# Performance work log

Measured on AMD Instinct MI355X. Metric: run time of the kernel, lower is better.

The kernel has to match this reference:

```python
import jax, jax.numpy as jnp
import numpy as np


def _upsample2x_axis_ac(arr, axis):
    size_in = arr.shape[axis]
    size_out = 2 * size_in
    pos = jnp.arange(size_out, dtype=arr.dtype) * ((size_in - 1) / (size_out - 1))
    i0 = jnp.clip(jnp.floor(pos).astype(jnp.int32), 0, size_in - 2)
    w = pos - i0.astype(arr.dtype)
    a = jnp.take(arr, i0, axis=axis)
    b = jnp.take(arr, i0 + 1, axis=axis)
    bshape = [1] * arr.ndim
    bshape[axis] = size_out
    w = w.reshape(bshape)
    return a * (1 - w) + b * w


def setup_inputs() -> dict:
    key = jax.random.key(0)
    k1, k2, k3, k4 = jax.random.split(key, 4)
    B, C, H, W = 8, 64, 256, 256
    Cr = 128  # readout channels (>= C, topk selects C of them)
    x = jax.random.normal(k1, (B, C, H, W), dtype=jnp.float32)
    readout = jax.random.normal(k2, (B, Cr, H // 2, W // 2), dtype=jnp.float32)
    weight = jax.random.normal(k3, (C, 2, 1, 1), dtype=jnp.float32) * 0.5
    bias = jax.random.normal(k4, (C,), dtype=jnp.float32) * 0.1
    return {"x": x, "readout": readout, "weight": weight, "bias": bias}


def reference(x, readout, weight, bias):
    B, C, H, W = x.shape
    r = _upsample2x_axis_ac(readout, 2)
    r = _upsample2x_axis_ac(r, 3)  # [B, Cr, H, W]
    # 2) topk channel selection by global-average score
    scores = r.mean(axis=(2, 3))  # [B, Cr]
    _, idx = jax.lax.top_k(scores, C)  # [B, C]
    r = jnp.take_along_axis(r, idx[:, :, None, None], axis=1)  # [B, C, H, W]
    # 3) interleave + grouped 1x1 conv (groups=C): group c sees channels
    #    (2c, 2c+1) = (x_c, r_c); equivalent to per-channel affine mix.
    w0 = weight[:, 0, 0, 0][None, :, None, None]
    w1 = weight[:, 1, 0, 0][None, :, None, None]
    gate = jax.nn.sigmoid(x * w0 + r * w1 + bias[None, :, None, None])
    # 4) sigmoid-gated blend
    return x * (1 - gate) + r * gate
```

## Files before the change

kernel.cpp:

```cpp
#include <hip/hip_runtime.h>
#include <math.h>

constexpr int B_   = 8;
constexpr int C_   = 64;
constexpr int H_   = 256;
constexpr int W_   = 256;
constexpr int CR_  = 128;
constexpr int HIN_ = 128;
constexpr int WIN_ = 128;

typedef float f4v __attribute__((ext_vector_type(4)));
typedef float f4u __attribute__((ext_vector_type(4), aligned(4)));

__device__ __forceinline__ float kScale() { return 127.0f / 255.0f; }

__global__ __launch_bounds__(256) void scores_kernel(
    const float* __restrict__ readout, float* __restrict__ scores)
{
    __shared__ float cw[HIN_];
    __shared__ float red[256];
    const int t  = threadIdx.x;
    const int bc = blockIdx.x;

    if (t < HIN_) {
        float acc = 0.0f;
        const float s = kScale();
        int jlo = 2 * t - 3; if (jlo < 0) jlo = 0;
        int jhi = 2 * t + 3; if (jhi > H_ - 1) jhi = H_ - 1;
        for (int j = jlo; j <= jhi; ++j) {
            float pos = j * s;
            int i0 = (int)pos;
            if (i0 > HIN_ - 2) i0 = HIN_ - 2;
            float w = pos - (float)i0;
            if (i0 == t)     acc += (1.0f - w);
            if (i0 + 1 == t) acc += w;
        }
        cw[t] = acc * (1.0f / 256.0f);
    }
    __syncthreads();

    const int c4 = t & 31;
    const int rg = t >> 5;
    const f4v* base = (const f4v*)(readout + (size_t)bc * HIN_ * WIN_);

    f4v a4 = (f4v){0.f, 0.f, 0.f, 0.f};
    const int i0r = rg * 16;
#pragma unroll 4
    for (int i = i0r; i < i0r + 16; ++i) {
        const float cwi = cw[i];
        f4v v = base[i * (WIN_ / 4) + c4];
        a4 += cwi * v;
    }
    red[t] = a4.x * cw[4 * c4 + 0] + a4.y * cw[4 * c4 + 1] +
             a4.z * cw[4 * c4 + 2] + a4.w * cw[4 * c4 + 3];
    __syncthreads();
    for (int off = 128; off > 0; off >>= 1) {
        if (t < off) red[t] += red[t + off];
        __syncthreads();
    }
    if (t == 0) scores[bc] = red[0];
}

__global__ __launch_bounds__(CR_) void topk_kernel(
    const float* __restrict__ scores, int* __restrict__ idx)
{
    __shared__ float s[CR_];
    const int t = threadIdx.x;
    const int b = blockIdx.x;
    s[t] = scores[b * CR_ + t];
    __syncthreads();
    const float mine = s[t];
    int rank = 0;
    for (int o = 0; o < CR_; ++o) {
        float so = s[o];
        rank += (so > mine) || (so == mine && o < t);
    }
    if (rank < C_) idx[b * C_ + rank] = t;
}

__device__ __forceinline__ float sel_a(f4u w, int d) {
    return d == 0 ? w[0] : (d == 1 ? w[1] : w[2]);
}
__device__ __forceinline__ float sel_b(f4u w, int d) {
    return d == 0 ? w[1] : (d == 1 ? w[2] : w[3]);
}

__global__ __launch_bounds__(256) void fuse_kernel(
    const float* __restrict__ x, const float* __restrict__ readout,
    const float* __restrict__ weight, const float* __restrict__ bias,
    const int* __restrict__ idx, float* __restrict__ out)
{
    constexpr int RPB = 16;
    const int gid  = blockIdx.x;
    const int bc   = gid >> 4;
    const int hblk = gid & 15;
    const int tid  = threadIdx.x;
    const int rgrp = tid >> 6;
    const int lane = tid & 63;
    const int b = bc >> 6;
    const int c = bc & 63;

    const int rc    = idx[b * C_ + c];
    const float w0  = weight[c * 2 + 0];
    const float w1  = weight[c * 2 + 1];
    const float bsv = bias[c];

    const float s = kScale();

    int   j0c[4];
    float wx[4];
    const int wbase = lane * 4;
#pragma unroll
    for (int k = 0; k < 4; ++k) {
        float wpos = (wbase + k) * s;
        int j0 = (int)wpos;
        if (j0 > WIN_ - 2) j0 = WIN_ - 2;
        wx[k]  = wpos - (float)j0;
        j0c[k] = j0;
    }
    int j00 = j0c[0];
    if (j00 > WIN_ - 4) j00 = WIN_ - 4;

    const float* rbase = readout + ((size_t)b * CR_ + rc) * HIN_ * WIN_;
    const float* xrow0 = x   + (((size_t)bc) * H_ + hblk * RPB + rgrp) * W_;
    float*       orow0 = out + (((size_t)bc) * H_ + hblk * RPB + rgrp) * W_;

#pragma unroll
    for (int rr = 0; rr < 4; ++rr) {
        const int h = hblk * RPB + rr * 4 + rgrp;
        float hpos = h * s;
        int i0 = (int)hpos;
        if (i0 > HIN_ - 2) i0 = HIN_ - 2;
        const float wy = hpos - (float)i0;

        const float* r0 = rbase + (size_t)i0 * WIN_;
        const float* r1 = r0 + WIN_;

        const f4v* xin = (const f4v*)(xrow0 + (size_t)(rr * 4) * W_);
        f4v*       oo  = (f4v*)      (orow0 + (size_t)(rr * 4) * W_);

        const f4v xv  = __builtin_nontemporal_load(&xin[lane]);
        const f4u w0v = *(const f4u*)(r0 + j00);
        const f4u w1v = *(const f4u*)(r1 + j00);

        const float xf[4] = {xv.x, xv.y, xv.z, xv.w};
        f4v ov;
#pragma unroll
        for (int k = 0; k < 4; ++k) {
            const int d = j0c[k] - j00;
            float ta = sel_a(w0v, d), tb = sel_b(w0v, d);
            float ba = sel_a(w1v, d), bb = sel_b(w1v, d);
            float top = ta + wx[k] * (tb - ta);
            float bot = ba + wx[k] * (bb - ba);
            float rv  = top + wy * (bot - top);

            float z = xf[k] * w0 + rv * w1 + bsv;
            float g = 1.0f / (1.0f + __expf(-z));
            ov[k] = xf[k] + g * (rv - xf[k]);
        }
        __builtin_nontemporal_store(ov, &oo[lane]);
    }
}

extern "C" void kernel_launch(void* const* d_in, const int* in_sizes, int n_in,
                              void* d_out, int out_size, void* d_ws, size_t ws_size,
                              hipStream_t stream)
{
    const float* x       = (const float*)d_in[0];
    const float* readout = (const float*)d_in[1];
    const float* weight  = (const float*)d_in[2];
    const float* bias    = (const float*)d_in[3];
    float* out = (float*)d_out;

    float* scores = (float*)d_ws;
    int*   idx    = (int*)((char*)d_ws + B_ * CR_ * sizeof(float));

    scores_kernel<<<B_ * CR_, 256, 0, stream>>>(readout, scores);
    topk_kernel<<<B_, CR_, 0, stream>>>(scores, idx);
    fuse_kernel<<<B_ * C_ * (H_ / 16), 256, 0, stream>>>(x, readout, weight, bias, idx, out);
}
```

Baseline: 278.6 us.

## Fuse scores, topk and blend into one cooperative kernel with grid syncs

Merges the three kernels into a single cooperative launch of 1024 blocks that use grid.sync between the score, top-k and blend phases. This removes two kernel launch gaps. Each block now processes 8 row tiles in the blend phase instead of one, which reduces parallelism from 8192 blocks to 1024. It also adds the cost of grid-wide barriers, and it falls back to the old three-kernel path if the cooperative launch fails.

```diff
diff --git a/kernel.cpp b/kernel.cpp
--- a/kernel.cpp
+++ b/kernel.cpp
@@ -1,5 +1,8 @@
 #include <hip/hip_runtime.h>
+#include <hip/hip_cooperative_groups.h>
 #include <math.h>
+
+namespace cg = cooperative_groups;
 
 constexpr int B_   = 8;
 constexpr int C_   = 64;
@@ -13,6 +16,162 @@
 typedef float f4u __attribute__((ext_vector_type(4), aligned(4)));
 
 __device__ __forceinline__ float kScale() { return 127.0f / 255.0f; }
+
+__device__ __forceinline__ float sel_a(f4u w, int d) {
+    return d == 0 ? w[0] : (d == 1 ? w[1] : w[2]);
+}
+__device__ __forceinline__ float sel_b(f4u w, int d) {
+    return d == 0 ? w[1] : (d == 1 ? w[2] : w[3]);
+}
+
+__global__ __launch_bounds__(256, 4) void mega_kernel(
+    const float* __restrict__ x, const float* __restrict__ readout,
+    const float* __restrict__ weight, const float* __restrict__ bias,
+    float* __restrict__ out, float* __restrict__ scores, int* __restrict__ idx)
+{
+    cg::grid_group grid = cg::this_grid();
+    const int t = threadIdx.x;
+
+    {
+        __shared__ float cw[HIN_];
+        __shared__ float red[256];
+        const int bc = blockIdx.x;
+
+        if (t < HIN_) {
+            float acc = 0.0f;
+            const float s = kScale();
+            int jlo = 2 * t - 3; if (jlo < 0) jlo = 0;
+            int jhi = 2 * t + 3; if (jhi > H_ - 1) jhi = H_ - 1;
+            for (int j = jlo; j <= jhi; ++j) {
+                float pos = j * s;
+                int i0 = (int)pos;
+                if (i0 > HIN_ - 2) i0 = HIN_ - 2;
+                float w = pos - (float)i0;
+                if (i0 == t)     acc += (1.0f - w);
+                if (i0 + 1 == t) acc += w;
+            }
+            cw[t] = acc * (1.0f / 256.0f);
+        }
+        __syncthreads();
+
+        const int c4 = t & 31;
+        const int rg = t >> 5;
+        const f4v* base = (const f4v*)(readout + (size_t)bc * HIN_ * WIN_);
+
+        f4v a4 = (f4v){0.f, 0.f, 0.f, 0.f};
+        const int i0r = rg * 16;
+#pragma unroll 4
+        for (int i = i0r; i < i0r + 16; ++i) {
+            const float cwi = cw[i];
+            f4v v = base[i * (WIN_ / 4) + c4];
+            a4 += cwi * v;
+        }
+        red[t] = a4.x * cw[4 * c4 + 0] + a4.y * cw[4 * c4 + 1] +
+                 a4.z * cw[4 * c4 + 2] + a4.w * cw[4 * c4 + 3];
+        __syncthreads();
+        for (int off = 128; off > 0; off >>= 1) {
+            if (t < off) red[t] += red[t + off];
+            __syncthreads();
+        }
+        if (t == 0) scores[bc] = red[0];
+    }
+
+    grid.sync();
+
+    if (blockIdx.x < B_) {
+        __shared__ float s[CR_];
+        const int b = blockIdx.x;
+        if (t < CR_) s[t] = scores[b * CR_ + t];
+        __syncthreads();
+        if (t < CR_) {
+            const float mine = s[t];
+            int rank = 0;
+            for (int o = 0; o < CR_; ++o) {
+                float so = s[o];
+                rank += (so > mine) || (so == mine && o < t);
+            }
+            if (rank < C_) idx[b * C_ + rank] = t;
+        }
+    }
+
+    grid.sync();
+
+    {
+        constexpr int RPB = 16;
+        const int tile0 = blockIdx.x * 8;
+        const int bc    = tile0 >> 4;
+        const int hblk0 = tile0 & 15;
+        const int rgrp  = t >> 6;
+        const int lane  = t & 63;
+        const int b = bc >> 6;
+        const int c = bc & 63;
+
+        const int rc    = idx[b * C_ + c];
+        const float w0  = weight[c * 2 + 0];
+        const float w1  = weight[c * 2 + 1];
+        const float bsv = bias[c];
+
+        const float s = kScale();
+
+        int   j0c[4];
+        float wx[4];
+        const int wbase = lane * 4;
+#pragma unroll
+        for (int k = 0; k < 4; ++k) {
+            float wpos = (wbase + k) * s;
+            int j0 = (int)wpos;
+            if (j0 > WIN_ - 2) j0 = WIN_ - 2;
+            wx[k]  = wpos - (float)j0;
+            j0c[k] = j0;
+        }
+        int j00 = j0c[0];
+        if (j00 > WIN_ - 4) j00 = WIN_ - 4;
+
+        const float* rbase = readout + ((size_t)b * CR_ + rc) * HIN_ * WIN_;
+
+        for (int kt = 0; kt < 8; ++kt) {
+            const int hblk = hblk0 + kt;
+            const float* xrow0 = x   + (((size_t)bc) * H_ + hblk * RPB + rgrp) * W_;
+            float*       orow0 = out + (((size_t)bc) * H_ + hblk * RPB + rgrp) * W_;
+
+#pragma unroll
+            for (int rr = 0; rr < 4; ++rr) {
+                const int h = hblk * RPB + rr * 4 + rgrp;
+                float hpos = h * s;
+                int i0 = (int)hpos;
+                if (i0 > HIN_ - 2) i0 = HIN_ - 2;
+                const float wy = hpos - (float)i0;
+
+                const float* r0 = rbase + (size_t)i0 * WIN_;
+                const float* r1 = r0 + WIN_;
+
+                const f4v* xin = (const f4v*)(xrow0 + (size_t)(rr * 4) * W_);
+                f4v*       oo  = (f4v*)      (orow0 + (size_t)(rr * 4) * W_);
+
+                const f4v xv  = __builtin_nontemporal_load(&xin[lane]);
+                const f4u w0v = *(const f4u*)(r0 + j00);
+                const f4u w1v = *(const f4u*)(r1 + j00);
+
+                const float xf[4] = {xv.x, xv.y, xv.z, xv.w};
+                f4v ov;
+#pragma unroll
+                for (int k = 0; k < 4; ++k) {
+                    const int d = j0c[k] - j00;
+                    float ta = sel_a(w0v, d), tb = sel_b(w0v, d);
+                    float ba = sel_a(w1v, d), bb = sel_b(w1v, d);
+                    float top = ta + wx[k] * (tb - ta);
+                    float bot = ba + wx[k] * (bb - ba);
+                    float rv  = top + wy * (bot - top);
+
+                    float z = xf[k] * w0 + rv * w1 + bsv;
+                    float g = 1.0f / (1.0f + __expf(-z));
+                    ov[k] = xf[k] + g * (rv - xf[k]);
+                }
+                __builtin_nontemporal_store(ov, &oo[lane]);
+            }
+        }
+    }
+}
 
 __global__ __launch_bounds__(256) void scores_kernel(
     const float* __restrict__ readout, float* __restrict__ scores)
@@ -78,13 +237,6 @@
     if (rank < C_) idx[b * C_ + rank] = t;
 }
 
-__device__ __forceinline__ float sel_a(f4u w, int d) {
-    return d == 0 ? w[0] : (d == 1 ? w[1] : w[2]);
-}
-__device__ __forceinline__ float sel_b(f4u w, int d) {
-    return d == 0 ? w[1] : (d == 1 ? w[2] : w[3]);
-}
-
 __global__ __launch_bounds__(256) void fuse_kernel(
     const float* __restrict__ x, const float* __restrict__ readout,
     const float* __restrict__ weight, const float* __restrict__ bias,
@@ -175,7 +327,13 @@
     float* scores = (float*)d_ws;
     int*   idx    = (int*)((char*)d_ws + B_ * CR_ * sizeof(float));
 
-    scores_kernel<<<B_ * CR_, 256, 0, stream>>>(readout, scores);
-    topk_kernel<<<B_, CR_, 0, stream>>>(scores, idx);
-    fuse_kernel<<<B_ * C_ * (H_ / 16), 256, 0, stream>>>(x, readout, weight, bias, idx, out);
-}
+    void* args[] = {(void*)&x, (void*)&readout, (void*)&weight, (void*)&bias,
+                    (void*)&out, (void*)&scores, (void*)&idx};
+    hipError_t err = hipLaunchCooperativeKernel(
+        (const void*)mega_kernel, dim3(B_ * CR_), dim3(256), args, 0, stream);
+    if (err != hipSuccess) {
+        scores_kernel<<<B_ * CR_, 256, 0, stream>>>(readout, scores);
+        topk_kernel<<<B_, CR_, 0, stream>>>(scores, idx);
+        fuse_kernel<<<B_ * C_ * (H_ / 16), 256, 0, stream>>>(x, readout, weight, bias, idx, out);
+    }
+}
```

Measured after the change: 499.5 us. 79.3% more time.
